# Optimization experiments

Measured on AMD Instinct MI355X. Metric: run time of the kernel, lower is better.

## Reference

```python
import jax, jax.numpy as jnp
import numpy as np

BCE_COEFF = 0.2
N_BOXES = 4194304


def setup_inputs() -> dict:
    key = jax.random.key(0)
    k1, k2, k3, k4, k5, k6, k7 = jax.random.split(key, 7)
    n = N_BOXES
    preds = jax.random.normal(k1, (n, 5), dtype=jnp.float32)
    # Build well-formed target boxes (x1<x2, y1<y2) with min size 0.1 in [0,1]
    x1 = jax.random.uniform(k2, (n,), dtype=jnp.float32) * 0.5
    y1 = jax.random.uniform(k3, (n,), dtype=jnp.float32) * 0.5
    w = 0.1 + 0.4 * jax.random.uniform(k4, (n,), dtype=jnp.float32)
    h = 0.1 + 0.4 * jax.random.uniform(k5, (n,), dtype=jnp.float32)
    lbl = jax.random.uniform(k6, (n,), dtype=jnp.float32)  # BCE targets in [0,1]
    target = jnp.stack([lbl, x1, y1, x1 + w, y1 + h], axis=1)
    return {"preds": preds, "target": target}


def _eiou_loss(p, t):
    # p, t: [n, 4] boxes (x1, y1, x2, y2); p already sigmoided
    pred_area = jnp.abs(p[:, 2] - p[:, 0]) * jnp.abs(p[:, 3] - p[:, 1])
    target_area = (t[:, 2] - t[:, 0]) * (t[:, 3] - t[:, 1])
    x_p1 = jnp.minimum(p[:, 2], p[:, 0])
    x_p2 = jnp.maximum(p[:, 2], p[:, 0])
    y_p1 = jnp.minimum(p[:, 1], p[:, 3])
    y_p2 = jnp.maximum(p[:, 1], p[:, 3])
    x1 = jnp.maximum(x_p1, t[:, 0])
    x2 = jnp.minimum(x_p2, t[:, 2])
    y1 = jnp.maximum(y_p1, t[:, 1])
    y2 = jnp.minimum(y_p2, t[:, 3])
    overlap = (x2 - x1) * (y2 - y1)
    overlap = jnp.where(overlap < 0, 0.0, overlap)  # faithful: clamp product only
    x1_c = jnp.minimum(x_p1, t[:, 0])
    x2_c = jnp.maximum(x_p2, t[:, 2])
    y1_c = jnp.minimum(y_p1, t[:, 1])
    y2_c = jnp.maximum(y_p2, t[:, 3])
    c_w = x2_c - x1_c
    c_h = y2_c - y1_c
    w = x_p2 - x_p1
    w_t = t[:, 2] - t[:, 0]
    h = y_p2 - y_p1
    h_t = t[:, 3] - t[:, 1]
    iou = overlap / (target_area + pred_area - overlap)
    cpx = (x_p2 + x_p1) * 0.5
    cpy = (y_p2 + y_p1) * 0.5
    ctx = (t[:, 2] + t[:, 0]) * 0.5
    cty = (t[:, 3] + t[:, 1]) * 0.5
    diag = c_w ** 2 + c_h ** 2
    center_part = ((cpx - ctx) ** 2 + (cpy - cty) ** 2) / diag
    width_part = (w - w_t) ** 2 / c_w ** 2
    height_part = (h - h_t) ** 2 / h_t ** 2  # faithful: h_t**2 denominator
    return 1.0 - (iou - (center_part + width_part + height_part))


def reference(preds, target):
    p_box = jax.nn.sigmoid(preds[:, 1:5])
    eiou = jnp.mean(_eiou_loss(p_box, target[:, 1:5]))
    # binary_cross_entropy_with_logits, mean reduction (numerically stable)
    x = preds[:, 0]
    y = target[:, 0]
    bce = jnp.mean(jnp.maximum(x, 0.0) - x * y + jnp.log1p(jnp.exp(-jnp.abs(x))))
    return BCE_COEFF * bce + eiou
```

## Files before the change

kernel.cpp:

```cpp
#include <hip/hip_runtime.h>

#define N_BOXES 4194304
#define BCE_COEFF 0.2f
#define BLOCK 256
#define CHUNK_BOXES 512
#define F4_PREDS (CHUNK_BOXES * 5 / 4)
#define NSLOTS 256

__global__ __launch_bounds__(BLOCK, 8) void eiou_bce_kernel(
        const float* __restrict__ preds,
        const float* __restrict__ target,
        float* __restrict__ slots) {
    __shared__ float s[CHUNK_BOXES * 5 * 2];
    float4* const s4 = reinterpret_cast<float4*>(s);

    const int t = threadIdx.x;
    const size_t f4Base = (size_t)blockIdx.x * (CHUNK_BOXES * 5 / 4);
    const float4* const p4 = reinterpret_cast<const float4*>(preds) + f4Base;
    const float4* const t4 = reinterpret_cast<const float4*>(target) + f4Base;

#pragma unroll
    for (int k = 0; k < 5; ++k) {
        const int idx = t + k * BLOCK;
        const float4* src = (idx < F4_PREDS) ? (p4 + idx)
                                             : (t4 + (idx - F4_PREDS));
        s4[idx] = *src;
    }
    __syncthreads();

    float acc = 0.0f;
#pragma unroll
    for (int k = 0; k < 2; ++k) {
        const int b = t + k * BLOCK;
        const float* __restrict__ P = &s[b * 5];
        const float* __restrict__ T = &s[CHUNK_BOXES * 5 + b * 5];

        const float x = P[0];
        const float y = T[0];
        const float p0 = __fdividef(1.0f, 1.0f + __expf(-P[1]));
        const float p1 = __fdividef(1.0f, 1.0f + __expf(-P[2]));
        const float p2 = __fdividef(1.0f, 1.0f + __expf(-P[3]));
        const float p3 = __fdividef(1.0f, 1.0f + __expf(-P[4]));
        const float t0 = T[1], t1 = T[2], t2 = T[3], t3 = T[4];

        const float pred_area   = fabsf(p2 - p0) * fabsf(p3 - p1);
        const float target_area = (t2 - t0) * (t3 - t1);

        const float xp1 = fminf(p2, p0), xp2 = fmaxf(p2, p0);
        const float yp1 = fminf(p1, p3), yp2 = fmaxf(p1, p3);

        const float x1 = fmaxf(xp1, t0), x2 = fminf(xp2, t2);
        const float y1 = fmaxf(yp1, t1), y2 = fminf(yp2, t3);

        float ov = (x2 - x1) * (y2 - y1);
        ov = (ov < 0.0f) ? 0.0f : ov;

        const float x1c = fminf(xp1, t0), x2c = fmaxf(xp2, t2);
        const float y1c = fminf(yp1, t1), y2c = fmaxf(yp2, t3);

        const float cw = x2c - x1c, ch = y2c - y1c;
        const float w  = xp2 - xp1, wt = t2 - t0;
        const float h  = yp2 - yp1, ht = t3 - t1;

        const float iou = __fdividef(ov, target_area + pred_area - ov);

        const float cpx = (xp2 + xp1) * 0.5f, cpy = (yp2 + yp1) * 0.5f;
        const float ctx = (t2 + t0) * 0.5f,   cty = (t3 + t1) * 0.5f;
        const float diag = cw * cw + ch * ch;
        const float dx = cpx - ctx, dy = cpy - cty;

        const float center_part = __fdividef(dx * dx + dy * dy, diag);
        const float dwv = w - wt;
        const float width_part  = __fdividef(dwv * dwv, cw * cw);
        const float dhv = h - ht;
        const float height_part = __fdividef(dhv * dhv, ht * ht);

        const float eiou = 1.0f - (iou - (center_part + width_part + height_part));

        const float bce = fmaxf(x, 0.0f) - x * y
                        + __logf(1.0f + __expf(-fabsf(x)));

        acc += BCE_COEFF * bce + eiou;
    }

#pragma unroll
    for (int off = 32; off > 0; off >>= 1)
        acc += __shfl_down(acc, off);

    __syncthreads();
    if ((t & 63) == 0) s[t >> 6] = acc;
    __syncthreads();
    if (t == 0) {
        const float bs = s[0] + s[1] + s[2] + s[3];
        atomicAdd(&slots[blockIdx.x & (NSLOTS - 1)], bs);
    }
}

__global__ __launch_bounds__(NSLOTS) void reduce_slots_kernel(
        const float* __restrict__ slots,
        float* __restrict__ out) {
    float v = slots[threadIdx.x];
#pragma unroll
    for (int off = 32; off > 0; off >>= 1)
        v += __shfl_down(v, off);

    __shared__ float ws[4];
    const int lane = threadIdx.x & 63;
    const int wid  = threadIdx.x >> 6;
    if (lane == 0) ws[wid] = v;
    __syncthreads();
    if (threadIdx.x == 0)
        out[0] = (ws[0] + ws[1] + ws[2] + ws[3]) * (1.0f / (float)N_BOXES);
}

extern "C" void kernel_launch(void* const* d_in, const int* in_sizes, int n_in,
                              void* d_out, int out_size, void* d_ws, size_t ws_size,
                              hipStream_t stream) {
    const float* preds  = (const float*)d_in[0];
    const float* target = (const float*)d_in[1];
    float* slots = (float*)d_ws;
    float* out   = (float*)d_out;

    hipMemsetAsync(slots, 0, NSLOTS * sizeof(float), stream);

    const int blocks = N_BOXES / CHUNK_BOXES;
    eiou_bce_kernel<<<blocks, BLOCK, 0, stream>>>(preds, target, slots);
    reduce_slots_kernel<<<1, NSLOTS, 0, stream>>>(slots, out);
}
```

Measured before the change: 38.80 us.

## Double-buffer global-to-LDS loads in persistent blocks and drop memset/atomics

The main kernel becomes persistent: 1024 blocks each loop over 8 chunks. The next chunk is prefetched into a second LDS buffer with direct global_load_lds while the current one is computed. Per-block sums are written to distinct slots instead of being atomically added, which removes the memset launch, and the final reducer reads 1024 slots as float4. The aim is to hide memory latency and cut launch and atomic overhead, at the cost of fewer blocks in flight and hand-written vmcnt waits.

```diff
diff --git a/kernel.cpp b/kernel.cpp
--- a/kernel.cpp
+++ b/kernel.cpp
@@ -1,105 +1,143 @@
 #include <hip/hip_runtime.h>
+#include <stdint.h>
 
 #define N_BOXES 4194304
 #define BCE_COEFF 0.2f
 #define BLOCK 256
-#define CHUNK_BOXES 512
-#define F4_PREDS (CHUNK_BOXES * 5 / 4)
-#define NSLOTS 256
+#define CHUNK 512
+#define F4_PER_INPUT 640
+#define F4_PER_CHUNK 1280
+#define NBLOCKS 1024
+#define CHUNKS_PER_BLOCK (N_BOXES / CHUNK / NBLOCKS)
 
-__global__ __launch_bounds__(BLOCK, 8) void eiou_bce_kernel(
+__device__ __forceinline__ void g2lds16(const float4* g, float4* l) {
+    __builtin_amdgcn_global_load_lds(
+        (const __attribute__((address_space(1))) void*)g,
+        (__attribute__((address_space(3))) void*)l,
+        16, 0, 0);
+}
+
+#define CFENCE() asm volatile("" ::: "memory")
+
+__global__ __launch_bounds__(BLOCK) void eiou_main(
         const float* __restrict__ preds,
         const float* __restrict__ target,
         float* __restrict__ slots) {
-    __shared__ float s[CHUNK_BOXES * 5 * 2];
-    float4* const s4 = reinterpret_cast<float4*>(s);
+    __shared__ float4 sbuf[2][F4_PER_CHUNK];
 
     const int t = threadIdx.x;
-    const size_t f4Base = (size_t)blockIdx.x * (CHUNK_BOXES * 5 / 4);
-    const float4* const p4 = reinterpret_cast<const float4*>(preds) + f4Base;
-    const float4* const t4 = reinterpret_cast<const float4*>(target) + f4Base;
+    const float4* const p4 = reinterpret_cast<const float4*>(preds);
+    const float4* const t4 = reinterpret_cast<const float4*>(target);
+    const int chunk0 = blockIdx.x * CHUNKS_PER_BLOCK;
 
+    {
+        const size_t pb = (size_t)chunk0 * F4_PER_INPUT;
 #pragma unroll
-    for (int k = 0; k < 5; ++k) {
-        const int idx = t + k * BLOCK;
-        const float4* src = (idx < F4_PREDS) ? (p4 + idx)
-                                             : (t4 + (idx - F4_PREDS));
-        s4[idx] = *src;
+        for (int k = 0; k < 5; ++k) {
+            const int idx = t + k * BLOCK;
+            const float4* src = (idx < F4_PER_INPUT) ? (p4 + pb + idx)
+                                                     : (t4 + pb + (idx - F4_PER_INPUT));
+            g2lds16(src, &sbuf[0][idx]);
+        }
     }
-    __syncthreads();
 
     float acc = 0.0f;
+
+    for (int c = 0; c < CHUNKS_PER_BLOCK; ++c) {
+        const int buf = c & 1;
+
+        if (c + 1 < CHUNKS_PER_BLOCK) {
+            const size_t pb = (size_t)(chunk0 + c + 1) * F4_PER_INPUT;
 #pragma unroll
-    for (int k = 0; k < 2; ++k) {
-        const int b = t + k * BLOCK;
-        const float* __restrict__ P = &s[b * 5];
-        const float* __restrict__ T = &s[CHUNK_BOXES * 5 + b * 5];
+            for (int k = 0; k < 5; ++k) {
+                const int idx = t + k * BLOCK;
+                const float4* src = (idx < F4_PER_INPUT) ? (p4 + pb + idx)
+                                                         : (t4 + pb + (idx - F4_PER_INPUT));
+                g2lds16(src, &sbuf[buf ^ 1][idx]);
+            }
+            asm volatile("s_waitcnt vmcnt(5)" ::: "memory");
+        } else {
+            asm volatile("s_waitcnt vmcnt(0)" ::: "memory");
+        }
+        CFENCE();
+        __builtin_amdgcn_s_barrier();
+        CFENCE();
 
-        const float x = P[0];
-        const float y = T[0];
-        const float p0 = __fdividef(1.0f, 1.0f + __expf(-P[1]));
-        const float p1 = __fdividef(1.0f, 1.0f + __expf(-P[2]));
-        const float p2 = __fdividef(1.0f, 1.0f + __expf(-P[3]));
-        const float p3 = __fdividef(1.0f, 1.0f + __expf(-P[4]));
-        const float t0 = T[1], t1 = T[2], t2 = T[3], t3 = T[4];
+        const float* __restrict__ s = reinterpret_cast<const float*>(&sbuf[buf][0]);
+#pragma unroll
+        for (int k = 0; k < 2; ++k) {
+            const int b = t + k * BLOCK;
+            const float* __restrict__ P = &s[b * 5];
+            const float* __restrict__ T = &s[CHUNK * 5 + b * 5];
 
-        const float pred_area   = fabsf(p2 - p0) * fabsf(p3 - p1);
-        const float target_area = (t2 - t0) * (t3 - t1);
+            const float x = P[0];
+            const float y = T[0];
+            const float p0 = __fdividef(1.0f, 1.0f + __expf(-P[1]));
+            const float p1 = __fdividef(1.0f, 1.0f + __expf(-P[2]));
+            const float p2 = __fdividef(1.0f, 1.0f + __expf(-P[3]));
+            const float p3 = __fdividef(1.0f, 1.0f + __expf(-P[4]));
+            const float t0 = T[1], t1 = T[2], t2 = T[3], t3 = T[4];
 
-        const float xp1 = fminf(p2, p0), xp2 = fmaxf(p2, p0);
-        const float yp1 = fminf(p1, p3), yp2 = fmaxf(p1, p3);
+            const float pred_area   = fabsf(p2 - p0) * fabsf(p3 - p1);
+            const float target_area = (t2 - t0) * (t3 - t1);
 
-        const float x1 = fmaxf(xp1, t0), x2 = fminf(xp2, t2);
-        const float y1 = fmaxf(yp1, t1), y2 = fminf(yp2, t3);
+            const float xp1 = fminf(p2, p0), xp2 = fmaxf(p2, p0);
+            const float yp1 = fminf(p1, p3), yp2 = fmaxf(p1, p3);
 
-        float ov = (x2 - x1) * (y2 - y1);
-        ov = (ov < 0.0f) ? 0.0f : ov;
+            const float x1 = fmaxf(xp1, t0), x2 = fminf(xp2, t2);
+            const float y1 = fmaxf(yp1, t1), y2 = fminf(yp2, t3);
 
-        const float x1c = fminf(xp1, t0), x2c = fmaxf(xp2, t2);
-        const float y1c = fminf(yp1, t1), y2c = fmaxf(yp2, t3);
+            float ov = (x2 - x1) * (y2 - y1);
+            ov = (ov < 0.0f) ? 0.0f : ov;
 
-        const float cw = x2c - x1c, ch = y2c - y1c;
-        const float w  = xp2 - xp1, wt = t2 - t0;
-        const float h  = yp2 - yp1, ht = t3 - t1;
+            const float x1c = fminf(xp1, t0), x2c = fmaxf(xp2, t2);
+            const float y1c = fminf(yp1, t1), y2c = fmaxf(yp2, t3);
 
-        const float iou = __fdividef(ov, target_area + pred_area - ov);
+            const float cw = x2c - x1c, ch = y2c - y1c;
+            const float w  = xp2 - xp1, wt = t2 - t0;
+            const float h  = yp2 - yp1, ht = t3 - t1;
 
-        const float cpx = (xp2 + xp1) * 0.5f, cpy = (yp2 + yp1) * 0.5f;
-        const float ctx = (t2 + t0) * 0.5f,   cty = (t3 + t1) * 0.5f;
-        const float diag = cw * cw + ch * ch;
-        const float dx = cpx - ctx, dy = cpy - cty;
+            const float iou = __fdividef(ov, target_area + pred_area - ov);
 
-        const float center_part = __fdividef(dx * dx + dy * dy, diag);
-        const float dwv = w - wt;
-        const float width_part  = __fdividef(dwv * dwv, cw * cw);
-        const float dhv = h - ht;
-        const float height_part = __fdividef(dhv * dhv, ht * ht);
+            const float cpx = (xp2 + xp1) * 0.5f, cpy = (yp2 + yp1) * 0.5f;
+            const float ctx = (t2 + t0) * 0.5f,   cty = (t3 + t1) * 0.5f;
+            const float diag = cw * cw + ch * ch;
+            const float dx = cpx - ctx, dy = cpy - cty;
 
-        const float eiou = 1.0f - (iou - (center_part + width_part + height_part));
+            const float center_part = __fdividef(dx * dx + dy * dy, diag);
+            const float dwv = w - wt;
+            const float width_part  = __fdividef(dwv * dwv, cw * cw);
+            const float dhv = h - ht;
+            const float height_part = __fdividef(dhv * dhv, ht * ht);
 
-        const float bce = fmaxf(x, 0.0f) - x * y
-                        + __logf(1.0f + __expf(-fabsf(x)));
+            const float eiou = 1.0f - (iou - (center_part + width_part + height_part));
 
-        acc += BCE_COEFF * bce + eiou;
+            const float bce = fmaxf(x, 0.0f) - x * y
+                            + __logf(1.0f + __expf(-fabsf(x)));
+
+            acc += BCE_COEFF * bce + eiou;
+        }
+
+        CFENCE();
+        __builtin_amdgcn_s_barrier();
+        CFENCE();
     }
 
 #pragma unroll
     for (int off = 32; off > 0; off >>= 1)
         acc += __shfl_down(acc, off);
 
+    float* sfl = reinterpret_cast<float*>(&sbuf[0][0]);
+    if ((t & 63) == 0) sfl[t >> 6] = acc;
     __syncthreads();
-    if ((t & 63) == 0) s[t >> 6] = acc;
-    __syncthreads();
-    if (t == 0) {
-        const float bs = s[0] + s[1] + s[2] + s[3];
-        atomicAdd(&slots[blockIdx.x & (NSLOTS - 1)], bs);
-    }
+    if (t == 0) slots[blockIdx.x] = (sfl[0] + sfl[1]) + (sfl[2] + sfl[3]);
 }
 
-__global__ __launch_bounds__(NSLOTS) void reduce_slots_kernel(
+__global__ __launch_bounds__(256) void reduce_slots_kernel(
         const float* __restrict__ slots,
         float* __restrict__ out) {
-    float v = slots[threadIdx.x];
+    const float4 v4 = reinterpret_cast<const float4*>(slots)[threadIdx.x];
+    float v = (v4.x + v4.y) + (v4.z + v4.w);
 #pragma unroll
     for (int off = 32; off > 0; off >>= 1)
         v += __shfl_down(v, off);
@@ -110,7 +148,7 @@
     if (lane == 0) ws[wid] = v;
     __syncthreads();
     if (threadIdx.x == 0)
-        out[0] = (ws[0] + ws[1] + ws[2] + ws[3]) * (1.0f / (float)N_BOXES);
+        out[0] = ((ws[0] + ws[1]) + (ws[2] + ws[3])) * (1.0f / (float)N_BOXES);
 }
 
 extern "C" void kernel_launch(void* const* d_in, const int* in_sizes, int n_in,
@@ -121,9 +159,6 @@
     float* slots = (float*)d_ws;
     float* out   = (float*)d_out;
 
-    hipMemsetAsync(slots, 0, NSLOTS * sizeof(float), stream);
-
-    const int blocks = N_BOXES / CHUNK_BOXES;
-    eiou_bce_kernel<<<blocks, BLOCK, 0, stream>>>(preds, target, slots);
-    reduce_slots_kernel<<<1, NSLOTS, 0, stream>>>(slots, out);
+    eiou_main<<<NBLOCKS, BLOCK, 0, stream>>>(preds, target, slots);
+    reduce_slots_kernel<<<1, 256, 0, stream>>>(slots, out);
 }
```

Measured after the change: 34.96 us. -9.9%, faster.
